# Optimization experiments

Measured on AMD Instinct MI355X. Metric: run time of the kernel, lower is better.

The kernel has to match this reference:

```python
import jax, jax.numpy as jnp
import numpy as np

B, S, QD, KVD = 4, 4096, 512, 512  # batch, seq_len (h*w), q_dim, kv_dim
N_HEAD = 1  # original torch view only works for n_head == 1


def setup_inputs() -> dict:
    key = jax.random.key(0)
    ks = jax.random.split(key, 12)
    s_q = 1.0 / np.sqrt(QD)
    s_kv = 1.0 / np.sqrt(KVD)
    return {
        "x": jax.random.normal(ks[0], (B, S, QD), jnp.float32),
        "y": jax.random.normal(ks[1], (B, S, KVD), jnp.float32),
        # torch nn.Linear weights: (out_features, in_features)
        "Wq": jax.random.normal(ks[2], (QD, QD), jnp.float32) * s_q,
        "bq": jnp.zeros((QD,), jnp.float32),
        "Wqv": jax.random.normal(ks[3], (QD, QD), jnp.float32) * s_q,
        "bqv": jnp.zeros((QD,), jnp.float32),
        "Wk": jax.random.normal(ks[4], (QD, KVD), jnp.float32) * s_kv,
        "bk": jnp.zeros((QD,), jnp.float32),
        "Wkv": jax.random.normal(ks[5], (QD, KVD), jnp.float32) * s_kv,
        "bkv": jnp.zeros((QD,), jnp.float32),
        "Wf": jax.random.normal(ks[6], (QD, QD), jnp.float32) * s_q,
        "bf": jnp.zeros((QD,), jnp.float32),
    }


def _linear(t, W, b):
    return jnp.einsum("bsd,od->bso", t, W) + b


def reference(x, y, Wq, bq, Wqv, bqv, Wk, bk, Wkv, bkv, Wf, bf):
    # projections
    q = _linear(x, Wq, bq)     # [B,S,D] query from target face
    qv = _linear(x, Wqv, bqv)  # [B,S,D] additive value stream from query side
    k = _linear(y, Wk, bk)     # [B,S,D]
    kv = _linear(y, Wkv, bkv)  # [B,S,D]
    # n_head == 1: the (B,S,1,D)->(B,1,S,D) transpose is a no-op reshape,
    # so attend directly over [B,S,D]. NOTE: no 1/sqrt(d) scaling (faithful).
    qk = jnp.einsum("bqd,bkd->bqk", q, k)          # [B,S,S]
    attn = jax.nn.softmax(qk, axis=-1)
    out = jnp.einsum("bqk,bkd->bqd", attn, kv) + qv  # fused AV + qv residual
    return _linear(out, Wf, bf)
```

## Files before the change

kernel.cpp:

```cpp
#include <hip/hip_runtime.h>

typedef _Float16 f16;
typedef _Float16 f16x8 __attribute__((ext_vector_type(8)));
typedef _Float16 f16x4 __attribute__((ext_vector_type(4)));
typedef float    f32x4 __attribute__((ext_vector_type(4)));

#define NB 4
#define SEQ 4096
#define DIM 512
#define MTOT (NB*SEQ)
#define NEL ((size_t)MTOT*DIM)

__global__ __launch_bounds__(256) void proj_gemm(
    const float* __restrict__ x, const float* __restrict__ y,
    const float* __restrict__ Wq, const float* __restrict__ bq,
    const float* __restrict__ Wqv, const float* __restrict__ bqv,
    const float* __restrict__ Wk, const float* __restrict__ bk,
    const float* __restrict__ Wkv, const float* __restrict__ bkv,
    f16* __restrict__ qh, f16* __restrict__ qvh,
    f16* __restrict__ kS, f16* __restrict__ vS)
{
    __shared__ __attribute__((aligned(16))) f16 a_lds[128][40];
    __shared__ __attribute__((aligned(16))) f16 b_lds[128][40];

    const int p = blockIdx.z;
    const float* A    = (p < 2) ? x : y;
    const float* W    = (p==0)?Wq:(p==1)?Wqv:(p==2)?Wk:Wkv;
    const float* bias = (p==0)?bq:(p==1)?bqv:(p==2)?bk:bkv;

    const int m0 = blockIdx.y * 128, n0 = blockIdx.x * 128;
    const int tid = threadIdx.x, lane = tid & 63, wv = tid >> 6;
    const int wm = wv >> 1, wn = wv & 1, mrow = lane & 15, qd = lane >> 4;

    f32x4 acc[4][4];
#pragma unroll
    for (int mt = 0; mt < 4; ++mt)
#pragma unroll
        for (int nt = 0; nt < 4; ++nt) acc[mt][nt] = (f32x4){0.f,0.f,0.f,0.f};

    float bv[4];
#pragma unroll
    for (int nt = 0; nt < 4; ++nt) bv[nt] = bias[n0 + wn*64 + nt*16 + mrow];

    for (int k0 = 0; k0 < DIM; k0 += 32) {
        __syncthreads();
#pragma unroll
        for (int i = 0; i < 4; ++i) {
            int c = i*256 + tid;
            int row = c >> 3, c4 = c & 7;
            float4 v = *(const float4*)(A + (size_t)(m0+row)*DIM + k0 + c4*4);
            f16x4 hh = { (f16)v.x, (f16)v.y, (f16)v.z, (f16)v.w };
            *(f16x4*)&a_lds[row][c4*4] = hh;
        }
#pragma unroll
        for (int i = 0; i < 4; ++i) {
            int c = i*256 + tid;
            int row = c >> 3, c4 = c & 7;
            float4 v = *(const float4*)(W + (size_t)(n0+row)*DIM + k0 + c4*4);
            f16x4 hh = { (f16)v.x, (f16)v.y, (f16)v.z, (f16)v.w };
            *(f16x4*)&b_lds[row][c4*4] = hh;
        }
        __syncthreads();
        f16x8 af[4], bfr[4];
#pragma unroll
        for (int mt = 0; mt < 4; ++mt) af[mt]  = *(const f16x8*)&a_lds[wm*64 + mt*16 + mrow][qd*8];
#pragma unroll
        for (int nt = 0; nt < 4; ++nt) bfr[nt] = *(const f16x8*)&b_lds[wn*64 + nt*16 + mrow][qd*8];
#pragma unroll
        for (int mt = 0; mt < 4; ++mt)
#pragma unroll
            for (int nt = 0; nt < 4; ++nt)
                acc[mt][nt] = __builtin_amdgcn_mfma_f32_16x16x32_f16(af[mt], bfr[nt], acc[mt][nt], 0,0,0);
    }

#pragma unroll
    for (int mt = 0; mt < 4; ++mt)
#pragma unroll
        for (int r = 0; r < 4; ++r) {
            int g = m0 + wm*64 + mt*16 + qd*4 + r;
#pragma unroll
            for (int nt = 0; nt < 4; ++nt) {
                int d = n0 + wn*64 + nt*16 + mrow;
                f16 val = (f16)(acc[mt][nt][r] + bv[nt]);
                if (p == 0) {
                    qh[(size_t)g*DIM + d] = val;
                } else if (p == 1) {
                    qvh[(size_t)g*DIM + d] = val;
                } else if (p == 2) {
                    int b = g >> 12, s = g & 4095;
                    int t = s >> 5, n = s & 31;
                    int chunk = d >> 8, ksl = (d >> 5) & 7, q = (d >> 3) & 3, j = d & 7;
                    size_t idx = (((size_t)((b*128 + t)*2048 + chunk*1024
                                   + n*32 + ((ksl*4 + q + n) & 31))) << 3) + j;
                    kS[idx] = val;
                } else {
                    int b = g >> 12, s = g & 4095;
                    int t = s >> 5, q = (s >> 3) & 3, j = s & 7;
                    int chunk = d >> 8, dl = d & 255;
                    size_t idx = (((size_t)((b*128 + t)*2048 + chunk*1024
                                   + dl*4 + ((q + (dl >> 1)) & 3))) << 3) + j;
                    vS[idx] = val;
                }
            }
        }
}

__global__ __launch_bounds__(256, 1) void attn_kernel(
    const f16* __restrict__ qh, const f16* __restrict__ kS,
    const f16* __restrict__ vS, const f16* __restrict__ qvh,
    f16* __restrict__ ao)
{
    __shared__ __attribute__((aligned(16))) f16 kbuf[2][16384];
    __shared__ __attribute__((aligned(16))) f16 vbuf[2][16384];
    __shared__ __attribute__((aligned(16))) f16 p_lds[4][16][40];

    const int xcd = blockIdx.x & 7;
    const int b   = xcd >> 1;
    const int qt  = (blockIdx.x >> 3) * 2 + (xcd & 1);
    const int tid = threadIdx.x, lane = tid & 63, w = tid >> 6;
    const int mrow = lane & 15, qd = lane >> 4;

    const f16* kSb = kS + ((size_t)b << 21);
    const f16* vSb = vS + ((size_t)b << 21);

    const size_t qrow = ((size_t)b*SEQ + qt*64 + w*16 + mrow) * DIM;
    f16x8 qf[16];
#pragma unroll
    for (int ks = 0; ks < 16; ++ks)
        qf[ks] = *(const f16x8*)(qh + qrow + ks*32 + qd*8);

    f32x4 o[32];
#pragma unroll
    for (int nt = 0; nt < 32; ++nt) o[nt] = (f32x4){0.f,0.f,0.f,0.f};
    f32x4 o_l = (f32x4){0.f,0.f,0.f,0.f};
    float m_i[4] = {-INFINITY,-INFINITY,-INFINITY,-INFINITY};
    const f16x8 ones = {(f16)1.f,(f16)1.f,(f16)1.f,(f16)1.f,
                        (f16)1.f,(f16)1.f,(f16)1.f,(f16)1.f};

    f16x8 sk[8], sv[8];
#pragma unroll
    for (int j = 0; j < 8; ++j) {
        sk[j] = *(const f16x8*)(kSb + (j*256 + tid)*8);
        sv[j] = *(const f16x8*)(vSb + (j*256 + tid)*8);
    }
#pragma unroll
    for (int j = 0; j < 8; ++j) {
        *(f16x8*)&kbuf[0][(j*256 + tid)*8] = sk[j];
        *(f16x8*)&vbuf[0][(j*256 + tid)*8] = sv[j];
    }
    __syncthreads();

    for (int i = 0; i < 128; ++i) {
        const int nxt = (i < 127) ? i + 1 : i;
        const f16* kt = kSb + (size_t)nxt*16384;
        const f16* vt = vSb + (size_t)nxt*16384;
#pragma unroll
        for (int j = 0; j < 8; ++j) {
            sk[j] = *(const f16x8*)(kt + (j*256 + tid)*8);
            sv[j] = *(const f16x8*)(vt + (j*256 + tid)*8);
        }

        const f16* kb = &kbuf[i & 1][0];
        const f16* vb = &vbuf[i & 1][0];

        f32x4 s0a = (f32x4){0.f,0.f,0.f,0.f}, s0b = s0a, s1a = s0a, s1b = s0a;
#pragma unroll
        for (int ksl = 0; ksl < 8; ++ksl) {
            int n0a = mrow, n1a = 16 + mrow;
            f16x8 kf0 = *(const f16x8*)&kb[(n0a*32 + ((ksl*4 + qd + n0a) & 31)) << 3];
            f16x8 kf1 = *(const f16x8*)&kb[(n1a*32 + ((ksl*4 + qd + n1a) & 31)) << 3];
            f16x8 kg0 = *(const f16x8*)&kb[(1024 + n0a*32 + ((ksl*4 + qd + n0a) & 31)) << 3];
            f16x8 kg1 = *(const f16x8*)&kb[(1024 + n1a*32 + ((ksl*4 + qd + n1a) & 31)) << 3];
            s0a = __builtin_amdgcn_mfma_f32_16x16x32_f16(qf[ksl],     kf0, s0a, 0,0,0);
            s1a = __builtin_amdgcn_mfma_f32_16x16x32_f16(qf[ksl],     kf1, s1a, 0,0,0);
            s0b = __builtin_amdgcn_mfma_f32_16x16x32_f16(qf[8 + ksl], kg0, s0b, 0,0,0);
            s1b = __builtin_amdgcn_mfma_f32_16x16x32_f16(qf[8 + ksl], kg1, s1b, 0,0,0);
        }
        f32x4 s0, s1;
#pragma unroll
        for (int rr = 0; rr < 4; ++rr) { s0[rr] = s0a[rr] + s0b[rr]; s1[rr] = s1a[rr] + s1b[rr]; }

        float alpha[4];
        bool changed = false;
#pragma unroll
        for (int rr = 0; rr < 4; ++rr) {
            float v = fmaxf(s0[rr], s1[rr]);
            v = fmaxf(v, __shfl_xor(v, 1));
            v = fmaxf(v, __shfl_xor(v, 2));
            v = fmaxf(v, __shfl_xor(v, 4));
            v = fmaxf(v, __shfl_xor(v, 8));
            float mn = fmaxf(m_i[rr], v);
            alpha[rr] = __expf(m_i[rr] - mn);
            if (mn > m_i[rr]) changed = true;
            m_i[rr] = mn;
            s0[rr] = __expf(s0[rr] - mn);
            s1[rr] = __expf(s1[rr] - mn);
        }
        if (__any(changed)) {
#pragma unroll
            for (int nt = 0; nt < 32; ++nt)
#pragma unroll
                for (int rr = 0; rr < 4; ++rr) o[nt][rr] *= alpha[rr];
#pragma unroll
            for (int rr = 0; rr < 4; ++rr) o_l[rr] *= alpha[rr];
        }

#pragma unroll
        for (int rr = 0; rr < 4; ++rr) {
            p_lds[w][qd*4 + rr][mrow]      = (f16)s0[rr];
            p_lds[w][qd*4 + rr][16 + mrow] = (f16)s1[rr];
        }
        f16x8 pf = *(const f16x8*)&p_lds[w][mrow][qd*8];
        o_l = __builtin_amdgcn_mfma_f32_16x16x32_f16(pf, ones, o_l, 0,0,0);

#pragma unroll
        for (int nt = 0; nt < 32; ++nt) {
            int d = nt*16 + mrow;
            int chunk = d >> 8, dl = d & 255;
            f16x8 vf = *(const f16x8*)&vb[(chunk*1024 + dl*4 + ((qd + (dl >> 1)) & 3)) << 3];
            o[nt] = __builtin_amdgcn_mfma_f32_16x16x32_f16(pf, vf, o[nt], 0,0,0);
        }

        f16* kw = &kbuf[(i + 1) & 1][0];
        f16* vw = &vbuf[(i + 1) & 1][0];
#pragma unroll
        for (int j = 0; j < 8; ++j) {
            *(f16x8*)&kw[(j*256 + tid)*8] = sk[j];
            *(f16x8*)&vw[(j*256 + tid)*8] = sv[j];
        }
        __syncthreads();
    }

    float inv_l[4];
#pragma unroll
    for (int rr = 0; rr < 4; ++rr) inv_l[rr] = 1.f / o_l[rr];
#pragma unroll
    for (int rr = 0; rr < 4; ++rr) {
        size_t grow = ((size_t)b*SEQ + qt*64 + w*16 + qd*4 + rr) * DIM;
#pragma unroll
        for (int nt = 0; nt < 32; ++nt) {
            int col = nt*16 + mrow;
            float val = o[nt][rr] * inv_l[rr] + (float)qvh[grow + col];
            ao[grow + col] = (f16)val;
        }
    }
}

__global__ __launch_bounds__(256) void final_gemm(
    const f16* __restrict__ ao, const float* __restrict__ Wf,
    const float* __restrict__ bf, float* __restrict__ out)
{
    __shared__ __attribute__((aligned(16))) f16 a_lds[128][40];
    __shared__ __attribute__((aligned(16))) f16 b_lds[128][40];

    const int m0 = blockIdx.y * 128, n0 = blockIdx.x * 128;
    const int tid = threadIdx.x, lane = tid & 63, wv = tid >> 6;
    const int wm = wv >> 1, wn = wv & 1, mrow = lane & 15, qd = lane >> 4;

    f32x4 acc[4][4];
#pragma unroll
    for (int mt = 0; mt < 4; ++mt)
#pragma unroll
        for (int nt = 0; nt < 4; ++nt) acc[mt][nt] = (f32x4){0.f,0.f,0.f,0.f};

    float bv[4];
#pragma unroll
    for (int nt = 0; nt < 4; ++nt) bv[nt] = bf[n0 + wn*64 + nt*16 + mrow];

    for (int k0 = 0; k0 < DIM; k0 += 32) {
        __syncthreads();
#pragma unroll
        for (int i = 0; i < 2; ++i) {
            int c = i*256 + tid;
            int row = c >> 2, c8 = c & 3;
            *(f16x8*)&a_lds[row][c8*8] =
                *(const f16x8*)(ao + (size_t)(m0+row)*DIM + k0 + c8*8);
        }
#pragma unroll
        for (int i = 0; i < 4; ++i) {
            int c = i*256 + tid;
            int row = c >> 3, c4 = c & 7;
            float4 v = *(const float4*)(Wf + (size_t)(n0+row)*DIM + k0 + c4*4);
            f16x4 hh = { (f16)v.x, (f16)v.y, (f16)v.z, (f16)v.w };
            *(f16x4*)&b_lds[row][c4*4] = hh;
        }
        __syncthreads();
        f16x8 af[4], bfr[4];
#pragma unroll
        for (int mt = 0; mt < 4; ++mt) af[mt]  = *(const f16x8*)&a_lds[wm*64 + mt*16 + mrow][qd*8];
#pragma unroll
        for (int nt = 0; nt < 4; ++nt) bfr[nt] = *(const f16x8*)&b_lds[wn*64 + nt*16 + mrow][qd*8];
#pragma unroll
        for (int mt = 0; mt < 4; ++mt)
#pragma unroll
            for (int nt = 0; nt < 4; ++nt)
                acc[mt][nt] = __builtin_amdgcn_mfma_f32_16x16x32_f16(af[mt], bfr[nt], acc[mt][nt], 0,0,0);
    }
#pragma unroll
    for (int mt = 0; mt < 4; ++mt)
#pragma unroll
        for (int r = 0; r < 4; ++r) {
            size_t grow = (size_t)(m0 + wm*64 + mt*16 + qd*4 + r) * DIM;
#pragma unroll
            for (int nt = 0; nt < 4; ++nt) {
                int col = n0 + wn*64 + nt*16 + mrow;
                out[grow + col] = acc[mt][nt][r] + bv[nt];
            }
        }
}

extern "C" void kernel_launch(void* const* d_in, const int* in_sizes, int n_in,
                              void* d_out, int out_size, void* d_ws, size_t ws_size,
                              hipStream_t stream)
{
    const float* x   = (const float*)d_in[0];
    const float* y   = (const float*)d_in[1];
    const float* Wq  = (const float*)d_in[2];
    const float* bq  = (const float*)d_in[3];
    const float* Wqv = (const float*)d_in[4];
    const float* bqv = (const float*)d_in[5];
    const float* Wk  = (const float*)d_in[6];
    const float* bk  = (const float*)d_in[7];
    const float* Wkv = (const float*)d_in[8];
    const float* bkv = (const float*)d_in[9];
    const float* Wf  = (const float*)d_in[10];
    const float* bf  = (const float*)d_in[11];
    float* out = (float*)d_out;

    f16* qh  = (f16*)d_ws;
    f16* qvh = qh  + NEL;
    f16* kS  = qvh + NEL;
    f16* vS  = kS  + NEL;
    f16* aob = vS  + NEL;

    proj_gemm<<<dim3(4, 128, 4), 256, 0, stream>>>(
        x, y, Wq, bq, Wqv, bqv, Wk, bk, Wkv, bkv, qh, qvh, kS, vS);
    attn_kernel<<<dim3(256), 256, 0, stream>>>(qh, kS, vS, qvh, aob);
    final_gemm<<<dim3(4, 128), 256, 0, stream>>>(aob, Wf, bf, out);
}
```

Measured before the change: 545.3 us.

## Split KV sequence across two wave groups per block with LDS softmax merge

The attention kernel now launches 512 threads, and two groups of four waves each process alternating KV tiles for the same 64 query rows. Their running max, sum and output accumulators are merged at the end through LDS. V tiles are loaded directly into LDS with global_load_lds, while K still goes through registers, and the double buffer now holds the tiles for the two halves rather than ping-pong stages. The goal is more waves in flight per CU to hide latency. The cost is extra syncs per iteration, no overlap of loads across iterations, and a final reduction step.

```diff
diff --git a/kernel.cpp b/kernel.cpp
--- a/kernel.cpp
+++ b/kernel.cpp
@@ -105,25 +105,38 @@
         }
 }
 
-__global__ __launch_bounds__(256, 1) void attn_kernel(
+__device__ __forceinline__ void gl_lds16(const f16* g, f16* l)
+{
+    __builtin_amdgcn_global_load_lds(
+        (const __attribute__((address_space(1))) void*)g,
+        (__attribute__((address_space(3))) void*)l, 16, 0, 0);
+}
+
+__global__ __launch_bounds__(512, 2) void attn_kernel(
     const f16* __restrict__ qh, const f16* __restrict__ kS,
     const f16* __restrict__ vS, const f16* __restrict__ qvh,
     f16* __restrict__ ao)
 {
     __shared__ __attribute__((aligned(16))) f16 kbuf[2][16384];
     __shared__ __attribute__((aligned(16))) f16 vbuf[2][16384];
-    __shared__ __attribute__((aligned(16))) f16 p_lds[4][16][40];
+    __shared__ __attribute__((aligned(16))) f16 p_lds[8][16][40];
+    __shared__ float mexch[8][4][4];
+    __shared__ float lexch[8][4][4];
 
     const int xcd = blockIdx.x & 7;
     const int b   = xcd >> 1;
     const int qt  = (blockIdx.x >> 3) * 2 + (xcd & 1);
     const int tid = threadIdx.x, lane = tid & 63, w = tid >> 6;
+    const int g = w & 3, half = w >> 2;
     const int mrow = lane & 15, qd = lane >> 4;
 
     const f16* kSb = kS + ((size_t)b << 21);
     const f16* vSb = vS + ((size_t)b << 21);
 
-    const size_t qrow = ((size_t)b*SEQ + qt*64 + w*16 + mrow) * DIM;
+    const f16* kb = &kbuf[half][0];
+    const f16* vb = &vbuf[half][0];
+
+    const size_t qrow = ((size_t)b*SEQ + qt*64 + g*16 + mrow) * DIM;
     f16x8 qf[16];
 #pragma unroll
     for (int ks = 0; ks < 16; ++ks)
@@ -137,31 +150,27 @@
     const f16x8 ones = {(f16)1.f,(f16)1.f,(f16)1.f,(f16)1.f,
                         (f16)1.f,(f16)1.f,(f16)1.f,(f16)1.f};
 
-    f16x8 sk[8], sv[8];
-#pragma unroll
-    for (int j = 0; j < 8; ++j) {
-        sk[j] = *(const f16x8*)(kSb + (j*256 + tid)*8);
-        sv[j] = *(const f16x8*)(vSb + (j*256 + tid)*8);
-    }
-#pragma unroll
-    for (int j = 0; j < 8; ++j) {
-        *(f16x8*)&kbuf[0][(j*256 + tid)*8] = sk[j];
-        *(f16x8*)&vbuf[0][(j*256 + tid)*8] = sv[j];
+#pragma unroll
+    for (int u = 0; u < 4; ++u) {
+        const int ubase = (u*8 + w) * 64;
+        gl_lds16(kSb + (size_t)(ubase + lane)*8,          (f16*)&kbuf[0][ubase*8]);
+        gl_lds16(kSb + (size_t)(2048 + ubase + lane)*8,   (f16*)&kbuf[1][ubase*8]);
+        gl_lds16(vSb + (size_t)(ubase + lane)*8,          (f16*)&vbuf[0][ubase*8]);
+        gl_lds16(vSb + (size_t)(2048 + ubase + lane)*8,   (f16*)&vbuf[1][ubase*8]);
     }
     __syncthreads();
 
-    for (int i = 0; i < 128; ++i) {
-        const int nxt = (i < 127) ? i + 1 : i;
-        const f16* kt = kSb + (size_t)nxt*16384;
-        const f16* vt = vSb + (size_t)nxt*16384;
-#pragma unroll
-        for (int j = 0; j < 8; ++j) {
-            sk[j] = *(const f16x8*)(kt + (j*256 + tid)*8);
-            sv[j] = *(const f16x8*)(vt + (j*256 + tid)*8);
-        }
-
-        const f16* kb = &kbuf[i & 1][0];
-        const f16* vb = &vbuf[i & 1][0];
+    f16x8 skA[4], skB[4];
+    for (int j = 0; j < 64; ++j) {
+        if (j < 63) {
+            const size_t t0 = (size_t)(2*j + 2) * 2048;
+#pragma unroll
+            for (int u = 0; u < 4; ++u) {
+                const int unit = u*512 + tid;
+                skA[u] = *(const f16x8*)(kSb + (t0 + unit)*8);
+                skB[u] = *(const f16x8*)(kSb + (t0 + 2048 + unit)*8);
+            }
+        }
 
         f32x4 s0a = (f32x4){0.f,0.f,0.f,0.f}, s0b = s0a, s1a = s0a, s1b = s0a;
 #pragma unroll
@@ -221,27 +230,71 @@
             o[nt] = __builtin_amdgcn_mfma_f32_16x16x32_f16(pf, vf, o[nt], 0,0,0);
         }
 
-        f16* kw = &kbuf[(i + 1) & 1][0];
-        f16* vw = &vbuf[(i + 1) & 1][0];
-#pragma unroll
-        for (int j = 0; j < 8; ++j) {
-            *(f16x8*)&kw[(j*256 + tid)*8] = sk[j];
-            *(f16x8*)&vw[(j*256 + tid)*8] = sv[j];
-        }
-        __syncthreads();
-    }
-
-    float inv_l[4];
-#pragma unroll
-    for (int rr = 0; rr < 4; ++rr) inv_l[rr] = 1.f / o_l[rr];
+        __syncthreads();
+        if (j < 63) {
+            const size_t t0 = (size_t)(2*j + 2) * 2048;
+#pragma unroll
+            for (int u = 0; u < 4; ++u) {
+                const int ubase = (u*8 + w) * 64;
+                gl_lds16(vSb + (t0 + ubase + lane)*8,        (f16*)&vbuf[0][ubase*8]);
+                gl_lds16(vSb + (t0 + 2048 + ubase + lane)*8, (f16*)&vbuf[1][ubase*8]);
+            }
+#pragma unroll
+            for (int u = 0; u < 4; ++u) {
+                const int unit = u*512 + tid;
+                *(f16x8*)&kbuf[0][unit*8] = skA[u];
+                *(f16x8*)&kbuf[1][unit*8] = skB[u];
+            }
+        }
+        __syncthreads();
+    }
+
+    if (mrow == 0) {
+#pragma unroll
+        for (int rr = 0; rr < 4; ++rr) {
+            mexch[w][qd][rr] = m_i[rr];
+            lexch[w][qd][rr] = o_l[rr];
+        }
+    }
+    __syncthreads();
+
+    const int pw = w ^ 4;
+    float al[4], l_tot[4];
 #pragma unroll
     for (int rr = 0; rr < 4; ++rr) {
-        size_t grow = ((size_t)b*SEQ + qt*64 + w*16 + qd*4 + rr) * DIM;
-#pragma unroll
-        for (int nt = 0; nt < 32; ++nt) {
-            int col = nt*16 + mrow;
-            float val = o[nt][rr] * inv_l[rr] + (float)qvh[grow + col];
-            ao[grow + col] = (f16)val;
+        float m_o = mexch[pw][qd][rr];
+        float l_o = lexch[pw][qd][rr];
+        float mm  = fmaxf(m_i[rr], m_o);
+        al[rr]    = __expf(m_i[rr] - mm);
+        l_tot[rr] = al[rr] * o_l[rr] + __expf(m_o - mm) * l_o;
+    }
+#pragma unroll
+    for (int nt = 0; nt < 32; ++nt)
+#pragma unroll
+        for (int rr = 0; rr < 4; ++rr) o[nt][rr] *= al[rr];
+
+    float* og = (g < 2) ? (float*)&kbuf[g][0] : (float*)&vbuf[g - 2][0];
+    if (half == 1) {
+#pragma unroll
+        for (int rr = 0; rr < 4; ++rr)
+#pragma unroll
+            for (int nt = 0; nt < 32; ++nt)
+                og[(qd*4 + rr)*512 + nt*16 + mrow] = o[nt][rr];
+    }
+    __syncthreads();
+
+    if (half == 0) {
+#pragma unroll
+        for (int rr = 0; rr < 4; ++rr) {
+            float inv_l = 1.f / l_tot[rr];
+            size_t grow = ((size_t)b*SEQ + qt*64 + g*16 + qd*4 + rr) * DIM;
+#pragma unroll
+            for (int nt = 0; nt < 32; ++nt) {
+                int col = nt*16 + mrow;
+                float val = (o[nt][rr] + og[(qd*4 + rr)*512 + col]) * inv_l
+                          + (float)qvh[grow + col];
+                ao[grow + col] = (f16)val;
+            }
         }
     }
 }
@@ -335,6 +388,6 @@
 
     proj_gemm<<<dim3(4, 128, 4), 256, 0, stream>>>(
         x, y, Wq, bq, Wqv, bqv, Wk, bk, Wkv, bkv, qh, qvh, kS, vS);
-    attn_kernel<<<dim3(256), 256, 0, stream>>>(qh, kS, vS, qvh, aob);
+    attn_kernel<<<dim3(256), 512, 0, stream>>>(qh, kS, vS, qvh, aob);
     final_gemm<<<dim3(4, 128), 256, 0, stream>>>(aob, Wf, bf, out);
 }
```

New measurement: 722.8 us. +32.5%, slower.

## Split head dimension across wave pairs and load K/V tiles via direct global-to-LDS

Applied to the files above, without the earlier changes.

Doubles the attention block to 512 threads, with two waves per query group each handling half of the 512-wide head dimension for both QK and PV, and exchanges partial scores through LDS. K/V tiles are now fetched with global_load_lds directly into the double buffer instead of staging through registers. This is meant to halve register usage and raise waves per CU to hide latency, at the cost of an extra barrier per tile and duplicated softmax work.

```diff
diff --git a/kernel.cpp b/kernel.cpp
--- a/kernel.cpp
+++ b/kernel.cpp
@@ -105,80 +105,92 @@
         }
 }
 
-__global__ __launch_bounds__(256, 1) void attn_kernel(
+__device__ __forceinline__ void gl_lds16(const f16* g, f16* l)
+{
+    __builtin_amdgcn_global_load_lds(
+        (const __attribute__((address_space(1))) void*)g,
+        (__attribute__((address_space(3))) void*)l, 16, 0, 0);
+}
+
+__global__ __launch_bounds__(512, 2) void attn_kernel(
     const f16* __restrict__ qh, const f16* __restrict__ kS,
     const f16* __restrict__ vS, const f16* __restrict__ qvh,
     f16* __restrict__ ao)
 {
     __shared__ __attribute__((aligned(16))) f16 kbuf[2][16384];
     __shared__ __attribute__((aligned(16))) f16 vbuf[2][16384];
-    __shared__ __attribute__((aligned(16))) f16 p_lds[4][16][40];
+    __shared__ __attribute__((aligned(16))) f16 p_lds[8][16][40];
+    __shared__ __attribute__((aligned(16))) f32x4 sx[4][2][2][64];
 
     const int xcd = blockIdx.x & 7;
     const int b   = xcd >> 1;
     const int qt  = (blockIdx.x >> 3) * 2 + (xcd & 1);
     const int tid = threadIdx.x, lane = tid & 63, w = tid >> 6;
+    const int qg = w & 3, h = w >> 2;
     const int mrow = lane & 15, qd = lane >> 4;
 
     const f16* kSb = kS + ((size_t)b << 21);
     const f16* vSb = vS + ((size_t)b << 21);
 
-    const size_t qrow = ((size_t)b*SEQ + qt*64 + w*16 + mrow) * DIM;
-    f16x8 qf[16];
-#pragma unroll
-    for (int ks = 0; ks < 16; ++ks)
-        qf[ks] = *(const f16x8*)(qh + qrow + ks*32 + qd*8);
-
-    f32x4 o[32];
-#pragma unroll
-    for (int nt = 0; nt < 32; ++nt) o[nt] = (f32x4){0.f,0.f,0.f,0.f};
+    const size_t qrow = ((size_t)b*SEQ + qt*64 + qg*16 + mrow) * DIM;
+    f16x8 qf[8];
+#pragma unroll
+    for (int i = 0; i < 8; ++i)
+        qf[i] = *(const f16x8*)(qh + qrow + (h*8 + i)*32 + qd*8);
+
+    f32x4 o[16];
+#pragma unroll
+    for (int nt = 0; nt < 16; ++nt) o[nt] = (f32x4){0.f,0.f,0.f,0.f};
     f32x4 o_l = (f32x4){0.f,0.f,0.f,0.f};
     float m_i[4] = {-INFINITY,-INFINITY,-INFINITY,-INFINITY};
     const f16x8 ones = {(f16)1.f,(f16)1.f,(f16)1.f,(f16)1.f,
                         (f16)1.f,(f16)1.f,(f16)1.f,(f16)1.f};
 
-    f16x8 sk[8], sv[8];
-#pragma unroll
-    for (int j = 0; j < 8; ++j) {
-        sk[j] = *(const f16x8*)(kSb + (j*256 + tid)*8);
-        sv[j] = *(const f16x8*)(vSb + (j*256 + tid)*8);
-    }
-#pragma unroll
-    for (int j = 0; j < 8; ++j) {
-        *(f16x8*)&kbuf[0][(j*256 + tid)*8] = sk[j];
-        *(f16x8*)&vbuf[0][(j*256 + tid)*8] = sv[j];
+#pragma unroll
+    for (int u = 0; u < 4; ++u) {
+        const int ubase = (u*8 + w) * 64;
+        gl_lds16(kSb + (size_t)(ubase + lane)*8, (f16*)&kbuf[0][ubase*8]);
+        gl_lds16(vSb + (size_t)(ubase + lane)*8, (f16*)&vbuf[0][ubase*8]);
     }
     __syncthreads();
 
-    for (int i = 0; i < 128; ++i) {
-        const int nxt = (i < 127) ? i + 1 : i;
-        const f16* kt = kSb + (size_t)nxt*16384;
-        const f16* vt = vSb + (size_t)nxt*16384;
-#pragma unroll
-        for (int j = 0; j < 8; ++j) {
-            sk[j] = *(const f16x8*)(kt + (j*256 + tid)*8);
-            sv[j] = *(const f16x8*)(vt + (j*256 + tid)*8);
-        }
-
-        const f16* kb = &kbuf[i & 1][0];
-        const f16* vb = &vbuf[i & 1][0];
-
-        f32x4 s0a = (f32x4){0.f,0.f,0.f,0.f}, s0b = s0a, s1a = s0a, s1b = s0a;
+    const int n0a = mrow, n1a = 16 + mrow;
+    const int cbase = h * 1024;
+
+    for (int j = 0; j < 128; ++j) {
+        const f16* kb = &kbuf[j & 1][0];
+        const f16* vb = &vbuf[j & 1][0];
+
+        if (j < 127) {
+            const size_t t0 = (size_t)(j + 1) * 2048;
+            f16* kd = &kbuf[(j + 1) & 1][0];
+            f16* vd = &vbuf[(j + 1) & 1][0];
+#pragma unroll
+            for (int u = 0; u < 4; ++u) {
+                const int ubase = (u*8 + w) * 64;
+                gl_lds16(kSb + (t0 + ubase + lane)*8, kd + ubase*8);
+                gl_lds16(vSb + (t0 + ubase + lane)*8, vd + ubase*8);
+            }
+        }
+
+        f32x4 s0 = (f32x4){0.f,0.f,0.f,0.f}, s1 = s0;
 #pragma unroll
         for (int ksl = 0; ksl < 8; ++ksl) {
-            int n0a = mrow, n1a = 16 + mrow;
-            f16x8 kf0 = *(const f16x8*)&kb[(n0a*32 + ((ksl*4 + qd + n0a) & 31)) << 3];
-            f16x8 kf1 = *(const f16x8*)&kb[(n1a*32 + ((ksl*4 + qd + n1a) & 31)) << 3];
-            f16x8 kg0 = *(const f16x8*)&kb[(1024 + n0a*32 + ((ksl*4 + qd + n0a) & 31)) << 3];
-            f16x8 kg1 = *(const f16x8*)&kb[(1024 + n1a*32 + ((ksl*4 + qd + n1a) & 31)) << 3];
-            s0a = __builtin_amdgcn_mfma_f32_16x16x32_f16(qf[ksl],     kf0, s0a, 0,0,0);
-            s1a = __builtin_amdgcn_mfma_f32_16x16x32_f16(qf[ksl],     kf1, s1a, 0,0,0);
-            s0b = __builtin_amdgcn_mfma_f32_16x16x32_f16(qf[8 + ksl], kg0, s0b, 0,0,0);
-            s1b = __builtin_amdgcn_mfma_f32_16x16x32_f16(qf[8 + ksl], kg1, s1b, 0,0,0);
-        }
-        f32x4 s0, s1;
-#pragma unroll
-        for (int rr = 0; rr < 4; ++rr) { s0[rr] = s0a[rr] + s0b[rr]; s1[rr] = s1a[rr] + s1b[rr]; }
+            f16x8 kf0 = *(const f16x8*)&kb[(cbase + n0a*32 + ((ksl*4 + qd + n0a) & 31)) << 3];
+            f16x8 kf1 = *(const f16x8*)&kb[(cbase + n1a*32 + ((ksl*4 + qd + n1a) & 31)) << 3];
+            s0 = __builtin_amdgcn_mfma_f32_16x16x32_f16(qf[ksl], kf0, s0, 0,0,0);
+            s1 = __builtin_amdgcn_mfma_f32_16x16x32_f16(qf[ksl], kf1, s1, 0,0,0);
+        }
+
+        sx[qg][h][0][lane] = s0;
+        sx[qg][h][1][lane] = s1;
+        __syncthreads();
+        {
+            f32x4 t0v = sx[qg][h ^ 1][0][lane];
+            f32x4 t1v = sx[qg][h ^ 1][1][lane];
+#pragma unroll
+            for (int rr = 0; rr < 4; ++rr) { s0[rr] += t0v[rr]; s1[rr] += t1v[rr]; }
+        }
 
         float alpha[4];
         bool changed = false;
@@ -198,7 +210,7 @@
         }
         if (__any(changed)) {
 #pragma unroll
-            for (int nt = 0; nt < 32; ++nt)
+            for (int nt = 0; nt < 16; ++nt)
 #pragma unroll
                 for (int rr = 0; rr < 4; ++rr) o[nt][rr] *= alpha[rr];
 #pragma unroll
@@ -214,33 +226,23 @@
         o_l = __builtin_amdgcn_mfma_f32_16x16x32_f16(pf, ones, o_l, 0,0,0);
 
 #pragma unroll
-        for (int nt = 0; nt < 32; ++nt) {
-            int d = nt*16 + mrow;
-            int chunk = d >> 8, dl = d & 255;
-            f16x8 vf = *(const f16x8*)&vb[(chunk*1024 + dl*4 + ((qd + (dl >> 1)) & 3)) << 3];
+        for (int nt = 0; nt < 16; ++nt) {
+            int dl = nt*16 + mrow;
+            f16x8 vf = *(const f16x8*)&vb[(cbase + dl*4 + ((qd + (dl >> 1)) & 3)) << 3];
             o[nt] = __builtin_amdgcn_mfma_f32_16x16x32_f16(pf, vf, o[nt], 0,0,0);
         }
 
-        f16* kw = &kbuf[(i + 1) & 1][0];
-        f16* vw = &vbuf[(i + 1) & 1][0];
-#pragma unroll
-        for (int j = 0; j < 8; ++j) {
-            *(f16x8*)&kw[(j*256 + tid)*8] = sk[j];
-            *(f16x8*)&vw[(j*256 + tid)*8] = sv[j];
-        }
-        __syncthreads();
-    }
-
-    float inv_l[4];
-#pragma unroll
-    for (int rr = 0; rr < 4; ++rr) inv_l[rr] = 1.f / o_l[rr];
+        __syncthreads();
+    }
+
 #pragma unroll
     for (int rr = 0; rr < 4; ++rr) {
-        size_t grow = ((size_t)b*SEQ + qt*64 + w*16 + qd*4 + rr) * DIM;
-#pragma unroll
-        for (int nt = 0; nt < 32; ++nt) {
+        float inv_l = 1.f / o_l[rr];
+        size_t grow = ((size_t)b*SEQ + qt*64 + qg*16 + qd*4 + rr) * DIM + h*256;
+#pragma unroll
+        for (int nt = 0; nt < 16; ++nt) {
             int col = nt*16 + mrow;
-            float val = o[nt][rr] * inv_l[rr] + (float)qvh[grow + col];
+            float val = o[nt][rr] * inv_l + (float)qvh[grow + col];
             ao[grow + col] = (f16)val;
         }
     }
@@ -335,6 +337,6 @@
 
     proj_gemm<<<dim3(4, 128, 4), 256, 0, stream>>>(
         x, y, Wq, bq, Wqv, bqv, Wk, bk, Wkv, bkv, qh, qvh, kS, vS);
-    attn_kernel<<<dim3(256), 256, 0, stream>>>(qh, kS, vS, qvh, aob);
+    attn_kernel<<<dim3(256), 512, 0, stream>>>(qh, kS, vS, qvh, aob);
     final_gemm<<<dim3(4, 128), 256, 0, stream>>>(aob, Wf, bf, out);
 }
```

New measurement: 536.6 us. About the same (-1.6%).

## Restructure attention with 32x32 MFMA, split-K waves, direct global K/V fragments

Applied to the files above, without the earlier changes.

Rewrites the attention kernel to use 512-thread blocks with 32x32x16 MFMA tiles. The QK^T reduction is split across waves over D halves and key-tile parity, and the partial scores are combined through LDS. K and V fragments are now loaded straight from global memory in a prepacked MFMA layout, replacing the LDS double buffer, and the projection kernel writes K and V in that new packed layout. The online softmax uses DPP row-max reductions and only rescales when the max grows by more than 8. This aims to raise MFMA efficiency and cut LDS traffic, at the cost of two barriers per iteration and more redundant global/L2 reads of K/V per block.

```diff
diff --git a/kernel.cpp b/kernel.cpp
--- a/kernel.cpp
+++ b/kernel.cpp
@@ -4,6 +4,7 @@
 typedef _Float16 f16x8 __attribute__((ext_vector_type(8)));
 typedef _Float16 f16x4 __attribute__((ext_vector_type(4)));
 typedef float    f32x4 __attribute__((ext_vector_type(4)));
+typedef float    f32x16 __attribute__((ext_vector_type(16)));
 
 #define NB 4
 #define SEQ 4096
@@ -18,7 +19,7 @@
     const float* __restrict__ Wk, const float* __restrict__ bk,
     const float* __restrict__ Wkv, const float* __restrict__ bkv,
     f16* __restrict__ qh, f16* __restrict__ qvh,
-    f16* __restrict__ kS, f16* __restrict__ vS)
+    f16* __restrict__ kP, f16* __restrict__ vP)
 {
     __shared__ __attribute__((aligned(16))) f16 a_lds[128][40];
     __shared__ __attribute__((aligned(16))) f16 b_lds[128][40];
@@ -87,161 +88,180 @@
                 } else if (p == 1) {
                     qvh[(size_t)g*DIM + d] = val;
                 } else if (p == 2) {
-                    int b = g >> 12, s = g & 4095;
-                    int t = s >> 5, n = s & 31;
-                    int chunk = d >> 8, ksl = (d >> 5) & 7, q = (d >> 3) & 3, j = d & 7;
-                    size_t idx = (((size_t)((b*128 + t)*2048 + chunk*1024
-                                   + n*32 + ((ksl*4 + q + n) & 31))) << 3) + j;
-                    kS[idx] = val;
+                    int gt = g >> 5, col = g & 31;
+                    int h2 = d >> 8, dl = d & 255;
+                    int s = dl >> 4, hi = (dl >> 3) & 1, j = d & 7;
+                    size_t u = ((size_t)(gt*2 + h2)*16 + s)*64 + hi*32 + col;
+                    kP[u*8 + j] = val;
                 } else {
-                    int b = g >> 12, s = g & 4095;
-                    int t = s >> 5, q = (s >> 3) & 3, j = s & 7;
-                    int chunk = d >> 8, dl = d & 255;
-                    size_t idx = (((size_t)((b*128 + t)*2048 + chunk*1024
-                                   + dl*4 + ((q + (dl >> 1)) & 3))) << 3) + j;
-                    vS[idx] = val;
+                    int gt = g >> 5, kvr = g & 31;
+                    int ks = kvr >> 4, hi = (kvr >> 3) & 1, jj = kvr & 7;
+                    int c32 = d >> 5, cl2 = d & 31;
+                    size_t u = ((size_t)(gt*16 + c32)*2 + ks)*64 + hi*32 + cl2;
+                    vP[u*8 + jj] = val;
                 }
             }
         }
 }
 
-__global__ __launch_bounds__(256, 1) void attn_kernel(
-    const f16* __restrict__ qh, const f16* __restrict__ kS,
-    const f16* __restrict__ vS, const f16* __restrict__ qvh,
+__device__ __forceinline__ float rowmax32(float v)
+{
+    int x;
+    x = __builtin_amdgcn_update_dpp(__builtin_bit_cast(int, v), __builtin_bit_cast(int, v), 0x111, 0xF, 0xF, false);
+    v = fmaxf(v, __builtin_bit_cast(float, x));
+    x = __builtin_amdgcn_update_dpp(__builtin_bit_cast(int, v), __builtin_bit_cast(int, v), 0x112, 0xF, 0xF, false);
+    v = fmaxf(v, __builtin_bit_cast(float, x));
+    x = __builtin_amdgcn_update_dpp(__builtin_bit_cast(int, v), __builtin_bit_cast(int, v), 0x114, 0xF, 0xF, false);
+    v = fmaxf(v, __builtin_bit_cast(float, x));
+    x = __builtin_amdgcn_update_dpp(__builtin_bit_cast(int, v), __builtin_bit_cast(int, v), 0x118, 0xF, 0xF, false);
+    v = fmaxf(v, __builtin_bit_cast(float, x));
+    float a = __builtin_bit_cast(float, __builtin_amdgcn_ds_swizzle(__builtin_bit_cast(int, v), 0x01E0));
+    float b = __builtin_bit_cast(float, __builtin_amdgcn_ds_swizzle(__builtin_bit_cast(int, v), 0x03E0));
+    return fmaxf(a, b);
+}
+
+__global__ __launch_bounds__(512, 2) void attn_kernel(
+    const f16* __restrict__ qh, const f16* __restrict__ kP,
+    const f16* __restrict__ vP, const f16* __restrict__ qvh,
     f16* __restrict__ ao)
 {
-    __shared__ __attribute__((aligned(16))) f16 kbuf[2][16384];
-    __shared__ __attribute__((aligned(16))) f16 vbuf[2][16384];
-    __shared__ __attribute__((aligned(16))) f16 p_lds[4][16][40];
+    __shared__ __attribute__((aligned(16))) f32x4 xch[2][4][4][64];
+    __shared__ __attribute__((aligned(16))) f16 plds[2][2][32][40];
 
     const int xcd = blockIdx.x & 7;
     const int b   = xcd >> 1;
     const int qt  = (blockIdx.x >> 3) * 2 + (xcd & 1);
     const int tid = threadIdx.x, lane = tid & 63, w = tid >> 6;
-    const int mrow = lane & 15, qd = lane >> 4;
-
-    const f16* kSb = kS + ((size_t)b << 21);
-    const f16* vSb = vS + ((size_t)b << 21);
-
-    const size_t qrow = ((size_t)b*SEQ + qt*64 + w*16 + mrow) * DIM;
+    const int qg = w & 1, h = (w >> 1) & 1, par = w >> 2;
+    const int slot = w >> 1;
+    const int dq = h*2 + par;
+    const int cl = lane & 31, lh = lane >> 5;
+
+    const size_t qoff = ((size_t)b*SEQ + qt*64 + qg*32 + cl)*DIM + h*256 + lh*8;
     f16x8 qf[16];
 #pragma unroll
-    for (int ks = 0; ks < 16; ++ks)
-        qf[ks] = *(const f16x8*)(qh + qrow + ks*32 + qd*8);
-
-    f32x4 o[32];
-#pragma unroll
-    for (int nt = 0; nt < 32; ++nt) o[nt] = (f32x4){0.f,0.f,0.f,0.f};
-    f32x4 o_l = (f32x4){0.f,0.f,0.f,0.f};
-    float m_i[4] = {-INFINITY,-INFINITY,-INFINITY,-INFINITY};
-    const f16x8 ones = {(f16)1.f,(f16)1.f,(f16)1.f,(f16)1.f,
-                        (f16)1.f,(f16)1.f,(f16)1.f,(f16)1.f};
-
-    f16x8 sk[8], sv[8];
-#pragma unroll
-    for (int j = 0; j < 8; ++j) {
-        sk[j] = *(const f16x8*)(kSb + (j*256 + tid)*8);
-        sv[j] = *(const f16x8*)(vSb + (j*256 + tid)*8);
-    }
-#pragma unroll
-    for (int j = 0; j < 8; ++j) {
-        *(f16x8*)&kbuf[0][(j*256 + tid)*8] = sk[j];
-        *(f16x8*)&vbuf[0][(j*256 + tid)*8] = sv[j];
-    }
-    __syncthreads();
-
-    for (int i = 0; i < 128; ++i) {
-        const int nxt = (i < 127) ? i + 1 : i;
-        const f16* kt = kSb + (size_t)nxt*16384;
-        const f16* vt = vSb + (size_t)nxt*16384;
-#pragma unroll
-        for (int j = 0; j < 8; ++j) {
-            sk[j] = *(const f16x8*)(kt + (j*256 + tid)*8);
-            sv[j] = *(const f16x8*)(vt + (j*256 + tid)*8);
-        }
-
-        const f16* kb = &kbuf[i & 1][0];
-        const f16* vb = &vbuf[i & 1][0];
-
-        f32x4 s0a = (f32x4){0.f,0.f,0.f,0.f}, s0b = s0a, s1a = s0a, s1b = s0a;
-#pragma unroll
-        for (int ksl = 0; ksl < 8; ++ksl) {
-            int n0a = mrow, n1a = 16 + mrow;
-            f16x8 kf0 = *(const f16x8*)&kb[(n0a*32 + ((ksl*4 + qd + n0a) & 31)) << 3];
-            f16x8 kf1 = *(const f16x8*)&kb[(n1a*32 + ((ksl*4 + qd + n1a) & 31)) << 3];
-            f16x8 kg0 = *(const f16x8*)&kb[(1024 + n0a*32 + ((ksl*4 + qd + n0a) & 31)) << 3];
-            f16x8 kg1 = *(const f16x8*)&kb[(1024 + n1a*32 + ((ksl*4 + qd + n1a) & 31)) << 3];
-            s0a = __builtin_amdgcn_mfma_f32_16x16x32_f16(qf[ksl],     kf0, s0a, 0,0,0);
-            s1a = __builtin_amdgcn_mfma_f32_16x16x32_f16(qf[ksl],     kf1, s1a, 0,0,0);
-            s0b = __builtin_amdgcn_mfma_f32_16x16x32_f16(qf[8 + ksl], kg0, s0b, 0,0,0);
-            s1b = __builtin_amdgcn_mfma_f32_16x16x32_f16(qf[8 + ksl], kg1, s1b, 0,0,0);
-        }
-        f32x4 s0, s1;
-#pragma unroll
-        for (int rr = 0; rr < 4; ++rr) { s0[rr] = s0a[rr] + s0b[rr]; s1[rr] = s1a[rr] + s1b[rr]; }
-
-        float alpha[4];
-        bool changed = false;
-#pragma unroll
-        for (int rr = 0; rr < 4; ++rr) {
-            float v = fmaxf(s0[rr], s1[rr]);
-            v = fmaxf(v, __shfl_xor(v, 1));
-            v = fmaxf(v, __shfl_xor(v, 2));
-            v = fmaxf(v, __shfl_xor(v, 4));
-            v = fmaxf(v, __shfl_xor(v, 8));
-            float mn = fmaxf(m_i[rr], v);
-            alpha[rr] = __expf(m_i[rr] - mn);
-            if (mn > m_i[rr]) changed = true;
-            m_i[rr] = mn;
-            s0[rr] = __expf(s0[rr] - mn);
-            s1[rr] = __expf(s1[rr] - mn);
-        }
-        if (__any(changed)) {
-#pragma unroll
-            for (int nt = 0; nt < 32; ++nt)
-#pragma unroll
-                for (int rr = 0; rr < 4; ++rr) o[nt][rr] *= alpha[rr];
-#pragma unroll
-            for (int rr = 0; rr < 4; ++rr) o_l[rr] *= alpha[rr];
-        }
-
-#pragma unroll
-        for (int rr = 0; rr < 4; ++rr) {
-            p_lds[w][qd*4 + rr][mrow]      = (f16)s0[rr];
-            p_lds[w][qd*4 + rr][16 + mrow] = (f16)s1[rr];
-        }
-        f16x8 pf = *(const f16x8*)&p_lds[w][mrow][qd*8];
-        o_l = __builtin_amdgcn_mfma_f32_16x16x32_f16(pf, ones, o_l, 0,0,0);
-
-#pragma unroll
-        for (int nt = 0; nt < 32; ++nt) {
-            int d = nt*16 + mrow;
-            int chunk = d >> 8, dl = d & 255;
-            f16x8 vf = *(const f16x8*)&vb[(chunk*1024 + dl*4 + ((qd + (dl >> 1)) & 3)) << 3];
-            o[nt] = __builtin_amdgcn_mfma_f32_16x16x32_f16(pf, vf, o[nt], 0,0,0);
-        }
-
-        f16* kw = &kbuf[(i + 1) & 1][0];
-        f16* vw = &vbuf[(i + 1) & 1][0];
-#pragma unroll
-        for (int j = 0; j < 8; ++j) {
-            *(f16x8*)&kw[(j*256 + tid)*8] = sk[j];
-            *(f16x8*)&vw[(j*256 + tid)*8] = sv[j];
-        }
-        __syncthreads();
-    }
-
-    float inv_l[4];
-#pragma unroll
-    for (int rr = 0; rr < 4; ++rr) inv_l[rr] = 1.f / o_l[rr];
-#pragma unroll
-    for (int rr = 0; rr < 4; ++rr) {
-        size_t grow = ((size_t)b*SEQ + qt*64 + w*16 + qd*4 + rr) * DIM;
-#pragma unroll
-        for (int nt = 0; nt < 32; ++nt) {
-            int col = nt*16 + mrow;
-            float val = o[nt][rr] * inv_l[rr] + (float)qvh[grow + col];
-            ao[grow + col] = (f16)val;
+    for (int s = 0; s < 16; ++s) qf[s] = *(const f16x8*)(qh + qoff + s*16);
+
+    const f16* kbase = kP + ((size_t)(b*128)*2 + h) * 8192;
+    const f16* vbase = vP + ((size_t)(b*128)*16 + dq*4) * 1024;
+
+    f32x16 o_[4];
+    f32x16 l16, m16;
+#pragma unroll
+    for (int i = 0; i < 16; ++i) {
+        o_[0][i] = 0.f; o_[1][i] = 0.f; o_[2][i] = 0.f; o_[3][i] = 0.f;
+        l16[i] = 0.f; m16[i] = -INFINITY;
+    }
+    const f16x8 onesv = {(f16)1.f,(f16)1.f,(f16)1.f,(f16)1.f,
+                         (f16)1.f,(f16)1.f,(f16)1.f,(f16)1.f};
+
+    for (int j = 0; j < 64; ++j) {
+        const f16* kt = kbase + (size_t)(2*j + par) * 16384;
+        f32x16 sacc;
+#pragma unroll
+        for (int i = 0; i < 16; ++i) sacc[i] = 0.f;
+#pragma unroll
+        for (int s = 0; s < 16; ++s) {
+            f16x8 kf = *(const f16x8*)(kt + s*512 + lane*8);
+            sacc = __builtin_amdgcn_mfma_f32_32x32x16_f16(qf[s], kf, sacc, 0,0,0);
+        }
+#pragma unroll
+        for (int ch = 0; ch < 4; ++ch) {
+            f32x4 t = { sacc[ch*4], sacc[ch*4+1], sacc[ch*4+2], sacc[ch*4+3] };
+            xch[qg][slot][ch][lane] = t;
+        }
+        __syncthreads();
+
+        f32x16 S0, S1;
+#pragma unroll
+        for (int ch = 0; ch < 4; ++ch) {
+            f32x4 p0 = xch[qg][0][ch][lane], p1 = xch[qg][1][ch][lane];
+            f32x4 p2 = xch[qg][2][ch][lane], p3 = xch[qg][3][ch][lane];
+#pragma unroll
+            for (int r = 0; r < 4; ++r) {
+                S0[ch*4+r] = p0[r] + p1[r];
+                S1[ch*4+r] = p2[r] + p3[r];
+            }
+        }
+
+        const f16* vt0 = vbase + (size_t)(2*j) * 16384;
+        f16x8 vs0[8];
+#pragma unroll
+        for (int c = 0; c < 4; ++c)
+#pragma unroll
+            for (int ks = 0; ks < 2; ++ks)
+                vs0[c*2+ks] = *(const f16x8*)(vt0 + c*1024 + ks*512 + lane*8);
+
+        f32x16 pm;
+#pragma unroll
+        for (int i = 0; i < 16; ++i) pm[i] = rowmax32(fmaxf(S0[i], S1[i]));
+        bool need = false;
+#pragma unroll
+        for (int i = 0; i < 16; ++i) need = need || (pm[i] > m16[i] + 8.f);
+        if (__any((int)need)) {
+#pragma unroll
+            for (int i = 0; i < 16; ++i) {
+                float mn = fmaxf(m16[i], pm[i]);
+                float al = __expf(m16[i] - mn);
+                m16[i] = mn;
+                o_[0][i] *= al; o_[1][i] *= al; o_[2][i] *= al; o_[3][i] *= al;
+                l16[i] *= al;
+            }
+        }
+        if (h == 0) {
+#pragma unroll
+            for (int i = 0; i < 16; ++i) {
+                float sv = (par == 0) ? S0[i] : S1[i];
+                int row = (i & 3) + 8*(i >> 2) + 4*lh;
+                plds[qg][par][row][cl] = (f16)__expf(sv - m16[i]);
+            }
+        }
+        __syncthreads();
+
+        f16x8 pa0 = *(const f16x8*)&plds[qg][0][cl][lh*8];
+        f16x8 pa1 = *(const f16x8*)&plds[qg][0][cl][16 + lh*8];
+        const f16* vt1 = vt0 + 16384;
+        f16x8 vsx[4];
+#pragma unroll
+        for (int ks = 0; ks < 2; ++ks) {
+            vsx[ks]   = *(const f16x8*)(vt1 + 0*1024 + ks*512 + lane*8);
+            vsx[2+ks] = *(const f16x8*)(vt1 + 1*1024 + ks*512 + lane*8);
+        }
+        l16 = __builtin_amdgcn_mfma_f32_32x32x16_f16(pa0, onesv, l16, 0,0,0);
+        l16 = __builtin_amdgcn_mfma_f32_32x32x16_f16(pa1, onesv, l16, 0,0,0);
+#pragma unroll
+        for (int c = 0; c < 4; ++c) {
+            o_[c] = __builtin_amdgcn_mfma_f32_32x32x16_f16(pa0, vs0[c*2],   o_[c], 0,0,0);
+            o_[c] = __builtin_amdgcn_mfma_f32_32x32x16_f16(pa1, vs0[c*2+1], o_[c], 0,0,0);
+        }
+        f16x8 pb0 = *(const f16x8*)&plds[qg][1][cl][lh*8];
+        f16x8 pb1 = *(const f16x8*)&plds[qg][1][cl][16 + lh*8];
+        l16 = __builtin_amdgcn_mfma_f32_32x32x16_f16(pb0, onesv, l16, 0,0,0);
+        l16 = __builtin_amdgcn_mfma_f32_32x32x16_f16(pb1, onesv, l16, 0,0,0);
+        o_[0] = __builtin_amdgcn_mfma_f32_32x32x16_f16(pb0, vsx[0], o_[0], 0,0,0);
+        o_[0] = __builtin_amdgcn_mfma_f32_32x32x16_f16(pb1, vsx[1], o_[0], 0,0,0);
+        o_[1] = __builtin_amdgcn_mfma_f32_32x32x16_f16(pb0, vsx[2], o_[1], 0,0,0);
+        o_[1] = __builtin_amdgcn_mfma_f32_32x32x16_f16(pb1, vsx[3], o_[1], 0,0,0);
+#pragma unroll
+        for (int ks = 0; ks < 2; ++ks) {
+            vsx[ks]   = *(const f16x8*)(vt1 + 2*1024 + ks*512 + lane*8);
+            vsx[2+ks] = *(const f16x8*)(vt1 + 3*1024 + ks*512 + lane*8);
+        }
+        o_[2] = __builtin_amdgcn_mfma_f32_32x32x16_f16(pb0, vsx[0], o_[2], 0,0,0);
+        o_[2] = __builtin_amdgcn_mfma_f32_32x32x16_f16(pb1, vsx[1], o_[2], 0,0,0);
+        o_[3] = __builtin_amdgcn_mfma_f32_32x32x16_f16(pb0, vsx[2], o_[3], 0,0,0);
+        o_[3] = __builtin_amdgcn_mfma_f32_32x32x16_f16(pb1, vsx[3], o_[3], 0,0,0);
+    }
+
+#pragma unroll
+    for (int i = 0; i < 16; ++i) {
+        float inv = 1.f / l16[i];
+        int row = (i & 3) + 8*(i >> 2) + 4*lh;
+        size_t grow = ((size_t)b*SEQ + qt*64 + qg*32 + row)*DIM + dq*128;
+#pragma unroll
+        for (int c = 0; c < 4; ++c) {
+            float val = o_[c][i]*inv + (float)qvh[grow + c*32 + cl];
+            ao[grow + c*32 + cl] = (f16)val;
         }
     }
 }
@@ -329,12 +349,12 @@
 
     f16* qh  = (f16*)d_ws;
     f16* qvh = qh  + NEL;
-    f16* kS  = qvh + NEL;
-    f16* vS  = kS  + NEL;
-    f16* aob = vS  + NEL;
+    f16* kP  = qvh + NEL;
+    f16* vP  = kP  + NEL;
+    f16* aob = vP  + NEL;
 
     proj_gemm<<<dim3(4, 128, 4), 256, 0, stream>>>(
-        x, y, Wq, bq, Wqv, bqv, Wk, bk, Wkv, bkv, qh, qvh, kS, vS);
-    attn_kernel<<<dim3(256), 256, 0, stream>>>(qh, kS, vS, qvh, aob);
+        x, y, Wq, bq, Wqv, bqv, Wk, bk, Wkv, bkv, qh, qvh, kP, vP);
+    attn_kernel<<<dim3(256), 512, 0, stream>>>(qh, kP, vP, qvh, aob);
     final_gemm<<<dim3(4, 128), 256, 0, stream>>>(aob, Wf, bf, out);
 }
```

Result: slower. 777.5 us (+42.6%).
